# Performance work log

Measured on AMD Instinct MI355X. Metric: run time of the kernel, lower is better.

## Reference

```python
import jax, jax.numpy as jnp
import numpy as np

IN_C, OUT_C, MAX_SIZE = 512, 256, 256
N = MAX_SIZE * MAX_SIZE  # 65536 nodes
E = MAX_SIZE * MAX_SIZE  # 65536 edges (before self loops)
NEG_SLOPE = 0.2


def setup_inputs() -> dict:
    key = jax.random.key(0)
    ks = jax.random.split(key, 12)
    s = 1.0 / np.sqrt(IN_C)
    so = 1.0 / np.sqrt(OUT_C)
    return {
        "x": jax.random.normal(ks[0], (N, IN_C), dtype=jnp.float32),
        "x_mask": jnp.ones((N,), dtype=bool),
        "edge_index": jax.random.randint(ks[1], (2, E), 0, N),
        "edge_mask": jnp.ones((E,), dtype=bool),
        "vaild_mask": jnp.ones((MAX_SIZE, MAX_SIZE), dtype=bool),
        # self-loop Linear
        "W_self": jax.random.uniform(ks[2], (IN_C, OUT_C), jnp.float32, -s, s),
        "b_self": jax.random.uniform(ks[3], (OUT_C,), jnp.float32, -s, s),
        # GATv2Conv params (heads=1)
        "W_l": jax.random.uniform(ks[4], (IN_C, OUT_C), jnp.float32, -s, s),
        "b_l": jnp.zeros((OUT_C,), jnp.float32),
        "W_r": jax.random.uniform(ks[5], (IN_C, OUT_C), jnp.float32, -s, s),
        "b_r": jnp.zeros((OUT_C,), jnp.float32),
        "att": jax.random.uniform(ks[6], (OUT_C,), jnp.float32, -so, so),
        "conv_bias": jnp.zeros((OUT_C,), jnp.float32),
        # sk classifier (out_channels -> 1)
        "W_cls": jax.random.uniform(ks[7], (OUT_C, 1), jnp.float32, -so, so),
        "b_cls": jax.random.uniform(ks[8], (1,), jnp.float32, -so, so),
    }


def _forward(x, edge_index, W_self, b_self, W_l, b_l, W_r, b_r, att,
             conv_bias, W_cls, b_cls):
    n = x.shape[0]
    # PyG GATv2Conv adds self-loops by default
    loops = jnp.arange(n, dtype=edge_index.dtype)
    src = jnp.concatenate([edge_index[0], loops])
    dst = jnp.concatenate([edge_index[1], loops])

    x_l = x @ W_l + b_l  # source-side transform (n, out)
    x_r = x @ W_r + b_r  # target-side transform (n, out)

    # per-edge GATv2 attention logits
    h = jax.nn.leaky_relu(x_l[src] + x_r[dst], NEG_SLOPE)  # (Etot, out)
    e = h @ att  # (Etot,)

    # segment softmax over incoming edges of each target node
    m = jnp.full((n,), -jnp.inf, dtype=e.dtype).at[dst].max(e)
    p = jnp.exp(e - m[dst])
    denom = jax.ops.segment_sum(p, dst, num_segments=n)
    alpha = p / denom[dst]

    x_neigh = jax.ops.segment_sum(alpha[:, None] * x_l[src], dst,
                                  num_segments=n) + conv_bias
    x_out = (x @ W_self + b_self) + x_neigh

    # sinkhorn-style row softmax channel (sk_channel=1, n1=n2=max_size)
    ms = MAX_SIZE
    sk = (x_out @ W_cls + b_cls).reshape(ms, ms)
    sk = jax.nn.softmax(sk, axis=-1)
    x_out = x_out + sk.reshape(-1, 1)
    # n1*n2 == max_size**2, so the padded output equals x_out
    return x_out


def reference(x, x_mask, edge_index, edge_mask, vaild_mask, W_self, b_self,
              W_l, b_l, W_r, b_r, att, conv_bias, W_cls, b_cls):
    # masks are all-True (fully valid case): x_valid = x, edges all kept
    return _forward(x, edge_index, W_self, b_self, W_l, b_l, W_r, b_r, att,
                    conv_bias, W_cls, b_cls)
```

## Files before the change

kernel.cpp:

```cpp
#include <hip/hip_runtime.h>
#include <hip/hip_bf16.h>
#include <stdint.h>

#define NNODE 65536
#define NEDGE 65536
#define ETOT  (NNODE + NEDGE)
#define INC   512
#define OUTC  256
#define NEG_SLOPE 0.2f
#define SLOTCAP 32

typedef __attribute__((ext_vector_type(8))) __bf16 bf16x8;
typedef __attribute__((ext_vector_type(4))) float f32x4;

__device__ __forceinline__ float b2f(unsigned short u) {
  return __uint_as_float(((unsigned int)u) << 16);
}
__device__ __forceinline__ unsigned short f2b(float f) {
  unsigned int u = __float_as_uint(f);
  u += 0x7fffu + ((u >> 16) & 1u);
  return (unsigned short)(u >> 16);
}
__device__ __forceinline__ unsigned int pk2(float lo, float hi) {
  return (unsigned int)f2b(lo) | ((unsigned int)f2b(hi) << 16);
}
__device__ __forceinline__ float lrelu(float v) {
  return v > 0.f ? v : NEG_SLOPE * v;
}

__global__ __launch_bounds__(256) void cvt_x_kernel(const float* __restrict__ x,
                                                    unsigned short* __restrict__ xb) {
  size_t i = ((size_t)blockIdx.x * 256 + threadIdx.x) * 8;
  float4 v0 = *(const float4*)(x + i);
  float4 v1 = *(const float4*)(x + i + 4);
  uint4 o;
  o.x = pk2(v0.x, v0.y);
  o.y = pk2(v0.z, v0.w);
  o.z = pk2(v1.x, v1.y);
  o.w = pk2(v1.z, v1.w);
  *(uint4*)(xb + i) = o;
}

__global__ __launch_bounds__(256) void prep_w_kernel(
    const float* __restrict__ Wl, const float* __restrict__ Wr, const float* __restrict__ Ws,
    const float* __restrict__ bl, const float* __restrict__ br, const float* __restrict__ bs,
    unsigned short* __restrict__ WT, float* __restrict__ bcat) {
  int i = blockIdx.x * 256 + threadIdx.x;
  if (i < 768 * 512) {
    int o = i >> 9, k = i & 511;
    float v;
    if (o < 256)      v = Wl[k * 256 + o];
    else if (o < 512) v = Wr[k * 256 + (o - 256)];
    else              v = Ws[k * 256 + (o - 512)];
    WT[i] = f2b(v);
  }
  if (i < 768) {
    bcat[i] = (i < 256) ? bl[i] : (i < 512 ? br[i - 256] : bs[i - 512]);
  }
}

__global__ __launch_bounds__(512) void gemm_kernel(
    const unsigned short* __restrict__ Xb,
    const unsigned short* __restrict__ WT,
    const float* __restrict__ bcat,
    unsigned short* __restrict__ xl,
    unsigned short* __restrict__ xr,
    unsigned short* __restrict__ xs) {
  __shared__ __align__(16) char smem[131072];
  unsigned short* sm = (unsigned short*)smem;

  const int wid = blockIdx.x;
  const int xcd = wid & 7;
  const int local = wid >> 3;
  const int by = local % 3;
  const int rowt = xcd * 32 + local / 3;
  const int rowBase = rowt * 256;
  const int colBase = by * 256;

  const int tid = threadIdx.x;
  const int lane = tid & 63;
  const int w = tid >> 6;
  const int wm = (w >> 2) * 128;
  const int wn = (w & 3) * 64;

  f32x4 acc[8][4] = {};

  auto stage = [&](int t, int buf) {
    const int kk = t * 32;
    const int q = tid;
    const int sl = q & 3;
#pragma unroll
    for (int l = 0; l < 2; ++l) {
      const int r = l * 128 + (q >> 2);
      const int slot = sl ^ ((r >> 1) & 3);
      const unsigned short* gA = Xb + (size_t)(rowBase + r) * 512 + kk + slot * 8;
      __builtin_amdgcn_global_load_lds(
          (const __attribute__((address_space(1))) void*)gA,
          (__attribute__((address_space(3))) void*)(sm + buf * 16384 + l * 4096 + q * 8), 16, 0, 0);
      const unsigned short* gB = WT + (size_t)(colBase + r) * 512 + kk + slot * 8;
      __builtin_amdgcn_global_load_lds(
          (const __attribute__((address_space(1))) void*)gB,
          (__attribute__((address_space(3))) void*)(sm + buf * 16384 + 8192 + l * 4096 + q * 8), 16, 0, 0);
    }
  };

  auto ldfrag = [&](int buf, bf16x8* fa, bf16x8* fb) {
    const unsigned short* As = sm + buf * 16384;
    const unsigned short* Bs = As + 8192;
    const int kq = lane >> 4;
#pragma unroll
    for (int m = 0; m < 8; ++m) {
      const int rA = wm + m * 16 + (lane & 15);
      fa[m] = *(const bf16x8*)&As[rA * 32 + ((kq ^ ((rA >> 1) & 3)) << 3)];
    }
#pragma unroll
    for (int n = 0; n < 4; ++n) {
      const int rB = wn + n * 16 + (lane & 15);
      fb[n] = *(const bf16x8*)&Bs[rB * 32 + ((kq ^ ((rB >> 1) & 3)) << 3)];
    }
  };

#define MFMA_BLOCK(FA, FB) { \
    __builtin_amdgcn_s_setprio(1); \
    _Pragma("unroll") \
    for (int m = 0; m < 8; ++m) \
      _Pragma("unroll") \
      for (int n = 0; n < 4; ++n) \
        acc[m][n] = __builtin_amdgcn_mfma_f32_16x16x32_bf16((FA)[m], (FB)[n], acc[m][n], 0, 0, 0); \
    __builtin_amdgcn_s_setprio(0); \
  }

  bf16x8 fa0[8], fb0[4], fa1[8], fb1[4];

  stage(0, 0);
  stage(1, 1);
  stage(2, 2);
  asm volatile("s_waitcnt vmcnt(8)" ::: "memory");
  __builtin_amdgcn_s_barrier();
  __builtin_amdgcn_sched_barrier(0);
  ldfrag(0, fa0, fb0);

#pragma unroll
  for (int t = 0; t < 16; ++t) {
    if (t <= 13)      asm volatile("s_waitcnt vmcnt(4)" ::: "memory");
    else if (t == 14) asm volatile("s_waitcnt vmcnt(0)" ::: "memory");
    if (t < 15) {
      __builtin_amdgcn_s_barrier();
      __builtin_amdgcn_sched_barrier(0);
    }
    if (t + 3 < 16) stage(t + 3, (t + 3) & 3);
    if ((t & 1) == 0) {
      if (t + 1 < 16) ldfrag((t + 1) & 3, fa1, fb1);
      MFMA_BLOCK(fa0, fb0);
    } else {
      if (t + 1 < 16) ldfrag((t + 1) & 3, fa0, fb0);
      MFMA_BLOCK(fa1, fb1);
    }
  }
#undef MFMA_BLOCK

  {
    unsigned short* dst = (by == 0) ? xl : (by == 1) ? xr : xs;
    float* eps = (float*)smem + w * 1088;
    float biasn[4];
#pragma unroll
    for (int n = 0; n < 4; ++n) biasn[n] = bcat[colBase + wn + n * 16 + (lane & 15)];
#pragma unroll
    for (int m = 0; m < 8; ++m) {
#pragma unroll
      for (int n = 0; n < 4; ++n)
#pragma unroll
        for (int j = 0; j < 4; ++j)
          eps[((lane >> 4) * 4 + j) * 68 + n * 16 + (lane & 15)] = acc[m][n][j] + biasn[n];
#pragma unroll
      for (int it = 0; it < 2; ++it) {
        const int r16 = it * 8 + (lane >> 3);
        const int c8 = (lane & 7) * 8;
        const float* srcp = eps + r16 * 68 + c8;
        float4 v0 = *(const float4*)srcp;
        float4 v1 = *(const float4*)(srcp + 4);
        uint4 o;
        o.x = pk2(v0.x, v0.y);
        o.y = pk2(v0.z, v0.w);
        o.z = pk2(v1.x, v1.y);
        o.w = pk2(v1.z, v1.w);
        *(uint4*)(dst + (size_t)(rowBase + wm + m * 16 + r16) * 256 + wn + c8) = o;
      }
    }
  }
}

__global__ __launch_bounds__(256) void edge_logit_kernel(
    const int* __restrict__ ei,
    const unsigned short* __restrict__ xl,
    const unsigned short* __restrict__ xr,
    const float* __restrict__ att,
    int* __restrict__ cnt,
    int* __restrict__ slot_src,
    float* __restrict__ slot_e) {
  const int j = blockIdx.x * 8 + (threadIdx.x >> 5);
  const int lane = threadIdx.x & 31;
  int src, dst;
  if (j < NEDGE) { src = ei[j]; dst = ei[NEDGE + j]; }
  else           { src = j - NEDGE; dst = src; }
  const int c = lane * 8;
  uint4 ul = *(const uint4*)(xl + (size_t)src * 256 + c);
  uint4 ur = *(const uint4*)(xr + (size_t)dst * 256 + c);
  float4 a0 = *(const float4*)(att + c);
  float4 a1 = *(const float4*)(att + c + 4);
  float s = lrelu(b2f((unsigned short)ul.x) + b2f((unsigned short)ur.x)) * a0.x
          + lrelu(b2f((unsigned short)(ul.x >> 16)) + b2f((unsigned short)(ur.x >> 16))) * a0.y
          + lrelu(b2f((unsigned short)ul.y) + b2f((unsigned short)ur.y)) * a0.z
          + lrelu(b2f((unsigned short)(ul.y >> 16)) + b2f((unsigned short)(ur.y >> 16))) * a0.w
          + lrelu(b2f((unsigned short)ul.z) + b2f((unsigned short)ur.z)) * a1.x
          + lrelu(b2f((unsigned short)(ul.z >> 16)) + b2f((unsigned short)(ur.z >> 16))) * a1.y
          + lrelu(b2f((unsigned short)ul.w) + b2f((unsigned short)ur.w)) * a1.z
          + lrelu(b2f((unsigned short)(ul.w >> 16)) + b2f((unsigned short)(ur.w >> 16))) * a1.w;
#pragma unroll
  for (int off = 16; off; off >>= 1) s += __shfl_xor(s, off);
  if (lane == 0) {
    const int pos = atomicAdd(&cnt[dst], 1);
    if (pos < SLOTCAP) {
      slot_src[dst * SLOTCAP + pos] = src;
      slot_e[dst * SLOTCAP + pos] = s;
    }
  }
}

__global__ __launch_bounds__(256) void node_kernel(
    const int* __restrict__ cnt,
    const int* __restrict__ slot_src, const float* __restrict__ slot_e,
    const unsigned short* __restrict__ xl,
    const unsigned short* __restrict__ xs,
    const float* __restrict__ conv_bias,
    float* __restrict__ out,
    const float* __restrict__ Wcls, const float* __restrict__ bcls,
    float* __restrict__ logits) {
  const int n = blockIdx.x * 4 + (threadIdx.x >> 6);
  const int lane = threadIdx.x & 63;
  const int base = n * SLOTCAP;
  const int deg = cnt[n];

  float m = -1e30f;
  for (int k = 0; k < deg; ++k) m = fmaxf(m, slot_e[base + k]);
  float denom = 0.f;
  for (int k = 0; k < deg; ++k) denom += __expf(slot_e[base + k] - m);
  const float inv = 1.f / denom;

  const int c = lane * 4;
  float4 accv = {0.f, 0.f, 0.f, 0.f};
  for (int k = 0; k < deg; ++k) {
    const float alpha = __expf(slot_e[base + k] - m) * inv;
    const int src = slot_src[base + k];
    ushort4 u = *(const ushort4*)(xl + (size_t)src * 256 + c);
    accv.x += alpha * b2f(u.x);
    accv.y += alpha * b2f(u.y);
    accv.z += alpha * b2f(u.z);
    accv.w += alpha * b2f(u.w);
  }
  ushort4 s4 = *(const ushort4*)(xs + (size_t)n * 256 + c);
  float4 cb = *(const float4*)(conv_bias + c);
  float4 cur;
  cur.x = b2f(s4.x) + accv.x + cb.x;
  cur.y = b2f(s4.y) + accv.y + cb.y;
  cur.z = b2f(s4.z) + accv.z + cb.z;
  cur.w = b2f(s4.w) + accv.w + cb.w;
  const size_t o = (size_t)n * 256 + c;
  *(float4*)(out + o) = cur;

  float4 wc = *(const float4*)(Wcls + c);
  float part = cur.x * wc.x + cur.y * wc.y + cur.z * wc.z + cur.w * wc.w;
#pragma unroll
  for (int off = 32; off; off >>= 1) part += __shfl_xor(part, off, 64);
  if (lane == 0) logits[n] = part + bcls[0];
}

__global__ __launch_bounds__(256) void sk_kernel(const float* __restrict__ logits,
                                                 float* __restrict__ out) {
  __shared__ float sv[256];
  __shared__ float red[256];
  const int r = blockIdx.x >> 2;
  const int q = blockIdx.x & 3;
  const int t = threadIdx.x;
  const float v = logits[r * 256 + t];
  red[t] = v;
  __syncthreads();
  for (int d = 128; d; d >>= 1) {
    if (t < d) red[t] = fmaxf(red[t], red[t + d]);
    __syncthreads();
  }
  const float mx = red[0];
  __syncthreads();
  const float p = __expf(v - mx);
  red[t] = p;
  __syncthreads();
  for (int d = 128; d; d >>= 1) {
    if (t < d) red[t] += red[t + d];
    __syncthreads();
  }
  const float sum = red[0];
  sv[t] = p / sum;
  __syncthreads();
  const size_t rowbase = (size_t)r * 256 * 256;
  for (int i = q * 64; i < q * 64 + 64; ++i) {
    out[rowbase + (size_t)i * 256 + t] += sv[i];
  }
}

extern "C" void kernel_launch(void* const* d_in, const int* in_sizes, int n_in,
                              void* d_out, int out_size, void* d_ws, size_t ws_size,
                              hipStream_t stream) {
  const float* x        = (const float*)d_in[0];
  const int*   ei       = (const int*)d_in[2];
  const float* W_self   = (const float*)d_in[5];
  const float* b_self   = (const float*)d_in[6];
  const float* W_l      = (const float*)d_in[7];
  const float* b_l      = (const float*)d_in[8];
  const float* W_r      = (const float*)d_in[9];
  const float* b_r      = (const float*)d_in[10];
  const float* att      = (const float*)d_in[11];
  const float* conv_bias= (const float*)d_in[12];
  const float* W_cls    = (const float*)d_in[13];
  const float* b_cls    = (const float*)d_in[14];
  float* out = (float*)d_out;

  char* ws = (char*)d_ws;
  size_t off = 0;
  auto alloc = [&](size_t bytes) {
    char* p = ws + off;
    off += (bytes + 255) & ~(size_t)255;
    return p;
  };
  unsigned short* xb   = (unsigned short*)alloc((size_t)NNODE * INC * 2);
  unsigned short* WT   = (unsigned short*)alloc((size_t)768 * 512 * 2);
  float*          bcat = (float*)alloc(768 * 4);
  unsigned short* xlb  = (unsigned short*)alloc((size_t)NNODE * OUTC * 2);
  unsigned short* xrb  = (unsigned short*)alloc((size_t)NNODE * OUTC * 2);
  unsigned short* xsb  = (unsigned short*)alloc((size_t)NNODE * OUTC * 2);
  int*            cnt  = (int*)alloc((size_t)NNODE * 4);
  float*          logits  = (float*)alloc((size_t)NNODE * 4);
  int*   slot_src = (int*)xb;
  float* slot_e   = (float*)(xb + (size_t)NNODE * SLOTCAP * 2);
  (void)ws_size; (void)in_sizes; (void)n_in; (void)out_size;

  hipMemsetAsync(cnt, 0, (size_t)NNODE * 4, stream);

  cvt_x_kernel<<<(NNODE * INC) / (256 * 8), 256, 0, stream>>>(x, xb);
  prep_w_kernel<<<(768 * 512 + 255) / 256, 256, 0, stream>>>(W_l, W_r, W_self, b_l, b_r, b_self, WT, bcat);
  gemm_kernel<<<768, 512, 0, stream>>>(xb, WT, bcat, xlb, xrb, xsb);
  edge_logit_kernel<<<ETOT / 8, 256, 0, stream>>>(ei, xlb, xrb, att, cnt, slot_src, slot_e);
  node_kernel<<<NNODE / 4, 256, 0, stream>>>(cnt, slot_src, slot_e, xlb, xsb, conv_bias,
                                             out, W_cls, b_cls, logits);
  sk_kernel<<<1024, 256, 0, stream>>>(logits, out);
}
```

Baseline: 209.4 us.

## Make GEMM persistent over all three weight column tiles and fold memset into convert

The GEMM grid shrinks from 768 to 256 blocks. Each block loops over the three 256-column outputs (x_l, x_r, x_s) with a 3-deep LDS ring that prefetches across column-tile boundaries, which removes two wave-startup and pipeline-fill phases per row tile. It also drops the separate hipMemsetAsync of the degree counters and zeroes them inside cvt_x_kernel instead. The risks are fewer blocks (256 on a 256-CU part, one wave of work), a shallower prefetch than the previous 4-buffer scheme, and a single fragment buffer with no double-buffered register fragments, so LDS-read latency may be exposed.

```diff
diff --git a/kernel.cpp b/kernel.cpp
--- a/kernel.cpp
+++ b/kernel.cpp
@@ -29,7 +29,9 @@
 }
 
 __global__ __launch_bounds__(256) void cvt_x_kernel(const float* __restrict__ x,
-                                                    unsigned short* __restrict__ xb) {
+                                                    unsigned short* __restrict__ xb,
+                                                    int* __restrict__ cnt) {
+  if (blockIdx.x < 256) cnt[blockIdx.x * 256 + threadIdx.x] = 0;
   size_t i = ((size_t)blockIdx.x * 256 + threadIdx.x) * 8;
   float4 v0 = *(const float4*)(x + i);
   float4 v1 = *(const float4*)(x + i + 4);
@@ -66,16 +68,14 @@
     unsigned short* __restrict__ xl,
     unsigned short* __restrict__ xr,
     unsigned short* __restrict__ xs) {
-  __shared__ __align__(16) char smem[131072];
-  unsigned short* sm = (unsigned short*)smem;
-
-  const int wid = blockIdx.x;
-  const int xcd = wid & 7;
-  const int local = wid >> 3;
-  const int by = local % 3;
-  const int rowt = xcd * 32 + local / 3;
+  __shared__ __align__(16) char smem[133120];
+  unsigned short* ring = (unsigned short*)smem;
+  float* epsall = (float*)(smem + 98304);
+
+  const int p = blockIdx.x;
+  const int xcd = p & 7;
+  const int rowt = xcd * 32 + (p >> 3);
   const int rowBase = rowt * 256;
-  const int colBase = by * 256;
 
   const int tid = threadIdx.x;
   const int lane = tid & 63;
@@ -83,10 +83,9 @@
   const int wm = (w >> 2) * 128;
   const int wn = (w & 3) * 64;
 
-  f32x4 acc[8][4] = {};
-
-  auto stage = [&](int t, int buf) {
-    const int kk = t * 32;
+  auto do_stage = [&](int by2, int t2, int buf) {
+    const int kk = t2 * 32;
+    const int cb2 = by2 * 256;
     const int q = tid;
     const int sl = q & 3;
 #pragma unroll
@@ -96,95 +95,87 @@
       const unsigned short* gA = Xb + (size_t)(rowBase + r) * 512 + kk + slot * 8;
       __builtin_amdgcn_global_load_lds(
           (const __attribute__((address_space(1))) void*)gA,
-          (__attribute__((address_space(3))) void*)(sm + buf * 16384 + l * 4096 + q * 8), 16, 0, 0);
-      const unsigned short* gB = WT + (size_t)(colBase + r) * 512 + kk + slot * 8;
+          (__attribute__((address_space(3))) void*)(ring + buf * 16384 + l * 4096 + q * 8), 16, 0, 0);
+      const unsigned short* gB = WT + (size_t)(cb2 + r) * 512 + kk + slot * 8;
       __builtin_amdgcn_global_load_lds(
           (const __attribute__((address_space(1))) void*)gB,
-          (__attribute__((address_space(3))) void*)(sm + buf * 16384 + 8192 + l * 4096 + q * 8), 16, 0, 0);
+          (__attribute__((address_space(3))) void*)(ring + buf * 16384 + 8192 + l * 4096 + q * 8), 16, 0, 0);
     }
   };
 
-  auto ldfrag = [&](int buf, bf16x8* fa, bf16x8* fb) {
-    const unsigned short* As = sm + buf * 16384;
-    const unsigned short* Bs = As + 8192;
-    const int kq = lane >> 4;
-#pragma unroll
-    for (int m = 0; m < 8; ++m) {
-      const int rA = wm + m * 16 + (lane & 15);
-      fa[m] = *(const bf16x8*)&As[rA * 32 + ((kq ^ ((rA >> 1) & 3)) << 3)];
-    }
-#pragma unroll
-    for (int n = 0; n < 4; ++n) {
-      const int rB = wn + n * 16 + (lane & 15);
-      fb[n] = *(const bf16x8*)&Bs[rB * 32 + ((kq ^ ((rB >> 1) & 3)) << 3)];
-    }
-  };
-
-#define MFMA_BLOCK(FA, FB) { \
-    __builtin_amdgcn_s_setprio(1); \
-    _Pragma("unroll") \
-    for (int m = 0; m < 8; ++m) \
-      _Pragma("unroll") \
-      for (int n = 0; n < 4; ++n) \
-        acc[m][n] = __builtin_amdgcn_mfma_f32_16x16x32_bf16((FA)[m], (FB)[n], acc[m][n], 0, 0, 0); \
-    __builtin_amdgcn_s_setprio(0); \
-  }
-
-  bf16x8 fa0[8], fb0[4], fa1[8], fb1[4];
-
-  stage(0, 0);
-  stage(1, 1);
-  stage(2, 2);
-  asm volatile("s_waitcnt vmcnt(8)" ::: "memory");
-  __builtin_amdgcn_s_barrier();
-  __builtin_amdgcn_sched_barrier(0);
-  ldfrag(0, fa0, fb0);
-
-#pragma unroll
-  for (int t = 0; t < 16; ++t) {
-    if (t <= 13)      asm volatile("s_waitcnt vmcnt(4)" ::: "memory");
-    else if (t == 14) asm volatile("s_waitcnt vmcnt(0)" ::: "memory");
-    if (t < 15) {
+  do_stage(0, 0, 0);
+  do_stage(0, 1, 1);
+
+  for (int by = 0; by < 3; ++by) {
+    f32x4 acc[8][4] = {};
+#pragma unroll
+    for (int t = 0; t < 16; ++t) {
+      if (t < 15) {
+        asm volatile("s_waitcnt vmcnt(4)" ::: "memory");
+      } else if (by < 2) {
+        asm volatile("s_waitcnt vmcnt(4)" ::: "memory");
+      } else {
+        asm volatile("s_waitcnt vmcnt(0)" ::: "memory");
+      }
       __builtin_amdgcn_s_barrier();
       __builtin_amdgcn_sched_barrier(0);
+
+      if (t <= 13)      do_stage(by, t + 2, (by + t + 2) % 3);
+      else if (by < 2)  do_stage(by + 1, t - 14, (by + t + 2) % 3);
+
+      {
+        const unsigned short* As = ring + ((by + t) % 3) * 16384;
+        const unsigned short* Bs = As + 8192;
+        const int kq = lane >> 4;
+        bf16x8 fa[8], fb[4];
+#pragma unroll
+        for (int m = 0; m < 8; ++m) {
+          const int rA = wm + m * 16 + (lane & 15);
+          fa[m] = *(const bf16x8*)&As[rA * 32 + ((kq ^ ((rA >> 1) & 3)) << 3)];
+        }
+#pragma unroll
+        for (int n = 0; n < 4; ++n) {
+          const int rB = wn + n * 16 + (lane & 15);
+          fb[n] = *(const bf16x8*)&Bs[rB * 32 + ((kq ^ ((rB >> 1) & 3)) << 3)];
+        }
+        __builtin_amdgcn_s_setprio(1);
+#pragma unroll
+        for (int m = 0; m < 8; ++m)
+#pragma unroll
+          for (int n = 0; n < 4; ++n)
+            acc[m][n] = __builtin_amdgcn_mfma_f32_16x16x32_bf16(fa[m], fb[n], acc[m][n], 0, 0, 0);
+        __builtin_amdgcn_s_setprio(0);
+      }
     }
-    if (t + 3 < 16) stage(t + 3, (t + 3) & 3);
-    if ((t & 1) == 0) {
-      if (t + 1 < 16) ldfrag((t + 1) & 3, fa1, fb1);
-      MFMA_BLOCK(fa0, fb0);
-    } else {
-      if (t + 1 < 16) ldfrag((t + 1) & 3, fa0, fb0);
-      MFMA_BLOCK(fa1, fb1);
-    }
-  }
-#undef MFMA_BLOCK
-
-  {
-    unsigned short* dst = (by == 0) ? xl : (by == 1) ? xr : xs;
-    float* eps = (float*)smem + w * 1088;
-    float biasn[4];
-#pragma unroll
-    for (int n = 0; n < 4; ++n) biasn[n] = bcat[colBase + wn + n * 16 + (lane & 15)];
-#pragma unroll
-    for (int m = 0; m < 8; ++m) {
-#pragma unroll
-      for (int n = 0; n < 4; ++n)
-#pragma unroll
-        for (int j = 0; j < 4; ++j)
-          eps[((lane >> 4) * 4 + j) * 68 + n * 16 + (lane & 15)] = acc[m][n][j] + biasn[n];
-#pragma unroll
-      for (int it = 0; it < 2; ++it) {
-        const int r16 = it * 8 + (lane >> 3);
-        const int c8 = (lane & 7) * 8;
-        const float* srcp = eps + r16 * 68 + c8;
-        float4 v0 = *(const float4*)srcp;
-        float4 v1 = *(const float4*)(srcp + 4);
-        uint4 o;
-        o.x = pk2(v0.x, v0.y);
-        o.y = pk2(v0.z, v0.w);
-        o.z = pk2(v1.x, v1.y);
-        o.w = pk2(v1.z, v1.w);
-        *(uint4*)(dst + (size_t)(rowBase + wm + m * 16 + r16) * 256 + wn + c8) = o;
+
+    {
+      unsigned short* dst = (by == 0) ? xl : (by == 1) ? xr : xs;
+      float* eps = epsall + w * 1088;
+      const int cb = by * 256;
+      float biasn[4];
+#pragma unroll
+      for (int n = 0; n < 4; ++n) biasn[n] = bcat[cb + wn + n * 16 + (lane & 15)];
+#pragma unroll
+      for (int m = 0; m < 8; ++m) {
+#pragma unroll
+        for (int n = 0; n < 4; ++n)
+#pragma unroll
+          for (int j = 0; j < 4; ++j)
+            eps[((lane >> 4) * 4 + j) * 68 + n * 16 + (lane & 15)] = acc[m][n][j] + biasn[n];
+#pragma unroll
+        for (int it = 0; it < 2; ++it) {
+          const int r16 = it * 8 + (lane >> 3);
+          const int c8 = (lane & 7) * 8;
+          const float* srcp = eps + r16 * 68 + c8;
+          float4 v0 = *(const float4*)srcp;
+          float4 v1 = *(const float4*)(srcp + 4);
+          uint4 o;
+          o.x = pk2(v0.x, v0.y);
+          o.y = pk2(v0.z, v0.w);
+          o.z = pk2(v1.x, v1.y);
+          o.w = pk2(v1.z, v1.w);
+          *(uint4*)(dst + (size_t)(rowBase + wm + m * 16 + r16) * 256 + wn + c8) = o;
+        }
       }
     }
   }
@@ -343,11 +334,9 @@
   float* slot_e   = (float*)(xb + (size_t)NNODE * SLOTCAP * 2);
   (void)ws_size; (void)in_sizes; (void)n_in; (void)out_size;
 
-  hipMemsetAsync(cnt, 0, (size_t)NNODE * 4, stream);
-
-  cvt_x_kernel<<<(NNODE * INC) / (256 * 8), 256, 0, stream>>>(x, xb);
+  cvt_x_kernel<<<(NNODE * INC) / (256 * 8), 256, 0, stream>>>(x, xb, cnt);
   prep_w_kernel<<<(768 * 512 + 255) / 256, 256, 0, stream>>>(W_l, W_r, W_self, b_l, b_r, b_self, WT, bcat);
-  gemm_kernel<<<768, 512, 0, stream>>>(xb, WT, bcat, xlb, xrb, xsb);
+  gemm_kernel<<<256, 512, 0, stream>>>(xb, WT, bcat, xlb, xrb, xsb);
   edge_logit_kernel<<<ETOT / 8, 256, 0, stream>>>(ei, xlb, xrb, att, cnt, slot_src, slot_e);
   node_kernel<<<NNODE / 4, 256, 0, stream>>>(cnt, slot_src, slot_e, xlb, xsb, conv_bias,
                                              out, W_cls, b_cls, logits);
```

Result: slower. 245.0 us (+17.0%).
